# Kernel optimization log

Hardware: AMD Instinct MI355X
Metric: run time of the kernel (lower is better)

Reference implementation:

```python
import jax, jax.numpy as jnp
import numpy as np

T, E = 16384, 1024   # frames, feature dim (WavLM-Large)
M, K = 8, 512        # number of kmeans models, clusters per model


def setup_inputs() -> dict:
    key = jax.random.key(0)
    k1, k2, k3 = jax.random.split(key, 3)
    emb = jax.random.normal(k1, (1, T, E), dtype=jnp.float32)
    centroids = jax.random.normal(k2, (M, K, E), dtype=jnp.float32)
    # per-frame random kmeans model choice (stride=1): replaces random.randint in the loop
    model_idx = jax.random.randint(k3, (T,), 0, M, dtype=jnp.int32)
    return {"emb": emb, "centroids": centroids, "model_idx": model_idx}


def reference(emb, centroids, model_idx):
    # emb: [1,T,E], centroids: [M,K,E], model_idx: [T] in [0,M)
    x = emb[0]  # [T,E]
    # squared euclidean distance from every frame to every centroid of every model
    # (argmin over squared dist == argmin over cdist)
    x_sq = jnp.sum(x * x, axis=-1)                      # [T]
    c_sq = jnp.sum(centroids * centroids, axis=-1)      # [M,K]
    dots = jnp.einsum('te,mke->tmk', x, centroids)      # [T,M,K]
    d_all = x_sq[:, None, None] - 2.0 * dots + c_sq[None, :, :]  # [T,M,K]
    # select the randomly chosen model's distances per frame
    d = jnp.take_along_axis(d_all, model_idx[:, None, None].astype(jnp.int32), axis=1)[:, 0, :]  # [T,K]
    codes = jnp.argmin(d, axis=-1)                      # [T]
    # embedding lookup: the quantizer's emb maps cluster id -> centroid vector
    out = centroids[model_idx, codes]                   # [T,E]
    return out[None]  # [1,T,E]
```

## Files before the change

kernel.cpp:

```cpp
#include <hip/hip_runtime.h>


#define T_FRAMES 16384
#define E_DIM    1024
#define M_MODELS 8
#define K_CLUST  512

#define FPB 32
#define NCH 8

typedef __bf16 bf16x8 __attribute__((ext_vector_type(8)));
typedef float  floatx16 __attribute__((ext_vector_type(16)));

__device__ __forceinline__ bf16x8 cvt8(const float4 a, const float4 b) {
  bf16x8 h;
  h[0] = (__bf16)a.x; h[1] = (__bf16)a.y; h[2] = (__bf16)a.z; h[3] = (__bf16)a.w;
  h[4] = (__bf16)b.x; h[5] = (__bf16)b.y; h[6] = (__bf16)b.z; h[7] = (__bf16)b.w;
  return h;
}

__global__ __launch_bounds__(256) void k_csq(const float* __restrict__ cent,
                                             double* __restrict__ csq64) {
  const int row = blockIdx.x * 4 + (threadIdx.x >> 6);
  const int lane = threadIdx.x & 63;
  const float* p = cent + (size_t)row * E_DIM;
  double s = 0.0;
#pragma unroll
  for (int i = 0; i < 16; ++i) {
    const float v = p[lane + i * 64];
    s += (double)v * (double)v;
  }
#pragma unroll
  for (int m = 32; m >= 1; m >>= 1) s += __shfl_xor(s, m, 64);
  if (lane == 0) csq64[row] = s;
}

__global__ __launch_bounds__(256) void k_cvt(const float* __restrict__ cent,
                                             float* __restrict__ out) {
  const int b = blockIdx.x;
  const int m = b >> 6;
  const int cg = (b >> 2) & 15;
  const int q = b & 3;
  const int tid = threadIdx.x;
  const int ci = tid & 31;
  const int gk0 = q * 32 + (tid >> 5) * 4;
  const int B32 = (m * 16 + cg) * 32;
  const float* src = cent + ((size_t)(m * K_CLUST + cg * 32 + ci)) * E_DIM;
#pragma unroll
  for (int j = 0; j < 4; ++j) {
    const int gk = gk0 + j;
    const float4 a = *(const float4*)(src + gk * 8);
    const float4 bb = *(const float4*)(src + gk * 8 + 4);
    const size_t foff = (size_t)(B32 + (gk >> 2)) * 1024 + 512 +
                        ((gk & 3) * 32 + ci) * 4;
    *(bf16x8*)(out + foff) = cvt8(a, bb);
  }
}

__global__ __launch_bounds__(256) void k_hist(const int* __restrict__ midx,
                                              int* __restrict__ hist) {
  __shared__ int h[M_MODELS * 33];
  const int tid = threadIdx.x;
  for (int i = tid; i < M_MODELS * 33; i += 256) h[i] = 0;
  __syncthreads();
  const int m = midx[blockIdx.x * 256 + tid];
  atomicAdd(&h[m * 33 + (tid & 31)], 1);
  __syncthreads();
  if (tid < M_MODELS) {
    int s = 0;
    for (int j = 0; j < 32; ++j) s += h[tid * 33 + j];
    hist[blockIdx.x * M_MODELS + tid] = s;
  }
}

__global__ __launch_bounds__(256) void k_scatter(const int* __restrict__ midx,
                                                 const int* __restrict__ hist,
                                                 int* __restrict__ order,
                                                 int* __restrict__ offs) {
  __shared__ int h2[64 * M_MODELS];
  __shared__ int cur[M_MODELS];
  const int tid = threadIdx.x;
  h2[tid] = hist[tid];
  h2[tid + 256] = hist[tid + 256];
  __syncthreads();
  if (tid < M_MODELS) {
    int tot_before = 0;
    for (int mp = 0; mp < tid; ++mp)
      for (int b = 0; b < 64; ++b) tot_before += h2[b * M_MODELS + mp];
    int prior = 0;
    for (int b = 0; b < (int)blockIdx.x; ++b) prior += h2[b * M_MODELS + tid];
    cur[tid] = tot_before + prior;
  }
  if (blockIdx.x == 0 && tid <= M_MODELS) {
    int o = 0;
    for (int mp = 0; mp < tid; ++mp)
      for (int b = 0; b < 64; ++b) o += h2[b * M_MODELS + mp];
    offs[tid] = o;
  }
  __syncthreads();
  const int f = blockIdx.x * 256 + tid;
  const int pos = atomicAdd(&cur[midx[f]], 1);
  order[pos] = f;
}

__global__ __launch_bounds__(256, 2) void k_dist(const float* __restrict__ emb,
                                                 const float* __restrict__ cent,
                                                 const double* __restrict__ csq64,
                                                 const int* __restrict__ order,
                                                 const int* __restrict__ offs,
                                                 float* __restrict__ out) {
  const int m = blockIdx.x;
  const int o0 = offs[m];
  const int cnt = offs[m + 1] - o0;
  const int start = blockIdx.y * FPB;
  if (start >= cnt) return;
  const int nvalid = min(FPB, cnt - start);

  __shared__ __align__(16) __bf16 A_l[2 * 16 * FPB * 8];
  __shared__ int rows_l[FPB];
  __shared__ float wmin_s[4][FPB];
  __shared__ int wcol_s[4][FPB];
  __shared__ float gmin_s[FPB];
  __shared__ int cnt_s[FPB];
  __shared__ int cand_s[FPB][32];

  const int tid = threadIdx.x;
  const int l = tid & 63;
  const int w = tid >> 6;
  const int ln = l & 31;
  const int lh = l >> 5;

  if (tid < FPB) rows_l[tid] = order[o0 + start + min(tid, nvalid - 1)];
  __syncthreads();

  const int s_row = tid & 31;
  const int s_gp = tid >> 5;
  const float4* emb4 = (const float4*)emb;
  const size_t arow4 = (size_t)rows_l[s_row] * (E_DIM / 4);

  float4 pa[4];
#pragma unroll
  for (int j = 0; j < 4; ++j) pa[j] = emb4[arow4 + s_gp * 4 + j];
  *(bf16x8*)(A_l + ((s_gp * 2 + 0) * FPB + s_row) * 8) = cvt8(pa[0], pa[1]);
  *(bf16x8*)(A_l + ((s_gp * 2 + 1) * FPB + s_row) * 8) = cvt8(pa[2], pa[3]);

  const char* bbase[4];
#pragma unroll
  for (int ct = 0; ct < 4; ++ct) {
    const int cg = w * 4 + ct;
    bbase[ct] = (const char*)out + (size_t)(m * 16 + cg) * 131072 + 2048 + l * 16;
  }
#define LOADB(ct, kb) (*(const bf16x8*)(bbase[ct] + (((kb) >> 1) << 12) + (((kb) & 1) << 10)))

  bf16x8 bR[4][4];
#pragma unroll
  for (int d = 0; d < 4; ++d)
#pragma unroll
    for (int ct = 0; ct < 4; ++ct) bR[d][ct] = LOADB(ct, d);

  floatx16 acc[4] = {};

  for (int c = 0; c < NCH; ++c) {
    __syncthreads();
    const int buf = (c & 1) * 16;
    if (c + 1 < NCH) {
#pragma unroll
      for (int j = 0; j < 4; ++j) pa[j] = emb4[arow4 + (c + 1) * 32 + s_gp * 4 + j];
    }
#pragma unroll
    for (int jj = 0; jj < 8; ++jj) {
      const int kb = c * 8 + jj;
      const int p = kb & 3;
      const bf16x8 a0 = *(const bf16x8*)(A_l + ((buf + jj * 2 + lh) * FPB + ln) * 8);
#pragma unroll
      for (int ct = 0; ct < 4; ++ct)
        acc[ct] = __builtin_amdgcn_mfma_f32_32x32x16_bf16(a0, bR[p][ct], acc[ct], 0, 0, 0);
      if (kb + 4 < 64) {
#pragma unroll
        for (int ct = 0; ct < 4; ++ct) bR[p][ct] = LOADB(ct, kb + 4);
      }
    }
    if (c + 1 < NCH) {
      const int nbuf = ((c + 1) & 1) * 16;
      *(bf16x8*)(A_l + ((nbuf + s_gp * 2 + 0) * FPB + s_row) * 8) = cvt8(pa[0], pa[1]);
      *(bf16x8*)(A_l + ((nbuf + s_gp * 2 + 1) * FPB + s_row) * 8) = cvt8(pa[2], pa[3]);
    }
  }
#undef LOADB

  float cs[4];
#pragma unroll
  for (int ct = 0; ct < 4; ++ct)
    cs[ct] = (float)csq64[m * K_CLUST + w * 128 + ct * 32 + ln];

#pragma unroll
  for (int r = 0; r < 16; ++r) {
    const int fr = (r & 3) + 8 * (r >> 2) + 4 * lh;
    float bm = cs[0] - 2.0f * acc[0][r];
    int bc = w * 128 + ln;
#pragma unroll
    for (int ct = 1; ct < 4; ++ct) {
      const float s = cs[ct] - 2.0f * acc[ct][r];
      if (s < bm) { bm = s; bc = w * 128 + ct * 32 + ln; }
    }
#pragma unroll
    for (int sh = 1; sh <= 16; sh <<= 1) {
      const float om = __shfl_xor(bm, sh, 64);
      const int oc = __shfl_xor(bc, sh, 64);
      if (om < bm || (om == bm && oc < bc)) { bm = om; bc = oc; }
    }
    if (ln == 0) { wmin_s[w][fr] = bm; wcol_s[w][fr] = bc; }
  }
  __syncthreads();

  if (tid < FPB) {
    float g = wmin_s[0][tid];
    int gc = wcol_s[0][tid];
#pragma unroll
    for (int w2 = 1; w2 < 4; ++w2) {
      const float v = wmin_s[w2][tid];
      const int vc = wcol_s[w2][tid];
      if (v < g || (v == g && vc < gc)) { g = v; gc = vc; }
    }
    gmin_s[tid] = g;
    cnt_s[tid] = 0;
  }
  __syncthreads();

#pragma unroll
  for (int r = 0; r < 16; ++r) {
    const int fr = (r & 3) + 8 * (r >> 2) + 4 * lh;
    const float thr = gmin_s[fr] + 3.0f;
#pragma unroll
    for (int ct = 0; ct < 4; ++ct) {
      const float s = cs[ct] - 2.0f * acc[ct][r];
      if (s < thr) {
        const int ix = atomicAdd(&cnt_s[fr], 1);
        if (ix < 32) cand_s[fr][ix] = w * 128 + ct * 32 + ln;
      }
    }
  }
  __syncthreads();

  for (int i = 0; i < 8; ++i) {
    const int f = w * 8 + i;
    const int t = rows_l[f];
    const int n = min(cnt_s[f], 32);
    int code;
    if (n == 1) {
      code = cand_s[f][0];
    } else {
      float4 xv[4];
#pragma unroll
      for (int q = 0; q < 4; ++q) xv[q] = emb4[(size_t)t * (E_DIM / 4) + q * 64 + l];
      double bd = 1e300;
      int bi = 1 << 30;
      for (int j = 0; j < n; ++j) {
        const int cc = cand_s[f][j];
        const float4* crow4 = (const float4*)(cent + ((size_t)(m * K_CLUST + cc)) * E_DIM);
        double s = 0.0;
#pragma unroll
        for (int q = 0; q < 4; ++q) {
          const float4 cv = crow4[q * 64 + l];
          s += (double)xv[q].x * cv.x + (double)xv[q].y * cv.y +
               (double)xv[q].z * cv.z + (double)xv[q].w * cv.w;
        }
#pragma unroll
        for (int sh = 32; sh >= 1; sh >>= 1) s += __shfl_xor(s, sh, 64);
        const double d = csq64[m * K_CLUST + cc] - 2.0 * s;
        if (d < bd || (d == bd && cc < bi)) { bd = d; bi = cc; }
      }
      code = bi;
    }
    if (l == 0) *(int*)(out + (size_t)t * E_DIM) = code;
  }
}

__global__ __launch_bounds__(256) void k_gather(const float* __restrict__ cent,
                                                const int* __restrict__ midx,
                                                float* __restrict__ out) {
  const int t = blockIdx.x * 4 + (threadIdx.x >> 6);
  const int l = threadIdx.x & 63;
  float* drow = out + (size_t)t * E_DIM;
  const int code = *(const int*)drow;
  const int m = midx[t];
  const float4* src = (const float4*)(cent + ((size_t)(m * K_CLUST + code)) * E_DIM);
  float4* dst = (float4*)drow;
#pragma unroll
  for (int q = 0; q < 4; ++q) dst[q * 64 + l] = src[q * 64 + l];
}

extern "C" void kernel_launch(void* const* d_in, const int* in_sizes, int n_in,
                              void* d_out, int out_size, void* d_ws, size_t ws_size,
                              hipStream_t stream) {
  const float* emb = (const float*)d_in[0];
  const float* cent = (const float*)d_in[1];
  const int* midx = (const int*)d_in[2];
  float* out = (float*)d_out;

  char* ws = (char*)d_ws;
  double* csq64 = (double*)(ws + 0);
  int* hist = (int*)(ws + 32768);
  int* offs = (int*)(ws + 34816);
  int* order = (int*)(ws + 34880);

  hipLaunchKernelGGL(k_cvt, dim3(512), dim3(256), 0, stream, cent, out);
  hipLaunchKernelGGL(k_csq, dim3(1024), dim3(256), 0, stream, cent, csq64);
  hipLaunchKernelGGL(k_hist, dim3(64), dim3(256), 0, stream, midx, hist);
  hipLaunchKernelGGL(k_scatter, dim3(64), dim3(256), 0, stream, midx, hist, order, offs);
  hipLaunchKernelGGL(k_dist, dim3(M_MODELS, 80), dim3(256), 0, stream,
                     emb, cent, csq64, order, offs, out);
  hipLaunchKernelGGL(k_gather, dim3(T_FRAMES / 4), dim3(256), 0, stream,
                     cent, midx, out);
}
```

Before: 206.2 us.

## Split distance kernel work across 8 waves with 64 clusters each

```diff
diff --git a/kernel.cpp b/kernel.cpp
--- a/kernel.cpp
+++ b/kernel.cpp
@@ -103,7 +103,7 @@
   order[pos] = f;
 }
 
-__global__ __launch_bounds__(256, 2) void k_dist(const float* __restrict__ emb,
+__global__ __launch_bounds__(512, 4) void k_dist(const float* __restrict__ emb,
                                                  const float* __restrict__ cent,
                                                  const double* __restrict__ csq64,
                                                  const int* __restrict__ order,
@@ -118,8 +118,8 @@
 
   __shared__ __align__(16) __bf16 A_l[2 * 16 * FPB * 8];
   __shared__ int rows_l[FPB];
-  __shared__ float wmin_s[4][FPB];
-  __shared__ int wcol_s[4][FPB];
+  __shared__ float wmin_s[8][FPB];
+  __shared__ int wcol_s[8][FPB];
   __shared__ float gmin_s[FPB];
   __shared__ int cnt_s[FPB];
   __shared__ int cand_s[FPB][32];
@@ -134,74 +134,70 @@
   __syncthreads();
 
   const int s_row = tid & 31;
-  const int s_gp = tid >> 5;
+  const int s_g = tid >> 5;
   const float4* emb4 = (const float4*)emb;
   const size_t arow4 = (size_t)rows_l[s_row] * (E_DIM / 4);
 
-  float4 pa[4];
-#pragma unroll
-  for (int j = 0; j < 4; ++j) pa[j] = emb4[arow4 + s_gp * 4 + j];
-  *(bf16x8*)(A_l + ((s_gp * 2 + 0) * FPB + s_row) * 8) = cvt8(pa[0], pa[1]);
-  *(bf16x8*)(A_l + ((s_gp * 2 + 1) * FPB + s_row) * 8) = cvt8(pa[2], pa[3]);
-
-  const char* bbase[4];
-#pragma unroll
-  for (int ct = 0; ct < 4; ++ct) {
-    const int cg = w * 4 + ct;
+  float4 pa[2];
+  pa[0] = emb4[arow4 + s_g * 2 + 0];
+  pa[1] = emb4[arow4 + s_g * 2 + 1];
+  *(bf16x8*)(A_l + ((s_g)*FPB + s_row) * 8) = cvt8(pa[0], pa[1]);
+
+  const char* bbase[2];
+#pragma unroll
+  for (int ct = 0; ct < 2; ++ct) {
+    const int cg = w * 2 + ct;
     bbase[ct] = (const char*)out + (size_t)(m * 16 + cg) * 131072 + 2048 + l * 16;
   }
 #define LOADB(ct, kb) (*(const bf16x8*)(bbase[ct] + (((kb) >> 1) << 12) + (((kb) & 1) << 10)))
 
-  bf16x8 bR[4][4];
+  bf16x8 bR[4][2];
 #pragma unroll
   for (int d = 0; d < 4; ++d)
 #pragma unroll
-    for (int ct = 0; ct < 4; ++ct) bR[d][ct] = LOADB(ct, d);
-
-  floatx16 acc[4] = {};
+    for (int ct = 0; ct < 2; ++ct) bR[d][ct] = LOADB(ct, d);
+
+  floatx16 acc[2] = {};
 
   for (int c = 0; c < NCH; ++c) {
     __syncthreads();
     const int buf = (c & 1) * 16;
     if (c + 1 < NCH) {
-#pragma unroll
-      for (int j = 0; j < 4; ++j) pa[j] = emb4[arow4 + (c + 1) * 32 + s_gp * 4 + j];
+      pa[0] = emb4[arow4 + (c + 1) * 32 + s_g * 2 + 0];
+      pa[1] = emb4[arow4 + (c + 1) * 32 + s_g * 2 + 1];
     }
 #pragma unroll
     for (int jj = 0; jj < 8; ++jj) {
       const int kb = c * 8 + jj;
       const int p = kb & 3;
       const bf16x8 a0 = *(const bf16x8*)(A_l + ((buf + jj * 2 + lh) * FPB + ln) * 8);
-#pragma unroll
-      for (int ct = 0; ct < 4; ++ct)
-        acc[ct] = __builtin_amdgcn_mfma_f32_32x32x16_bf16(a0, bR[p][ct], acc[ct], 0, 0, 0);
+      acc[0] = __builtin_amdgcn_mfma_f32_32x32x16_bf16(a0, bR[p][0], acc[0], 0, 0, 0);
+      acc[1] = __builtin_amdgcn_mfma_f32_32x32x16_bf16(a0, bR[p][1], acc[1], 0, 0, 0);
       if (kb + 4 < 64) {
-#pragma unroll
-        for (int ct = 0; ct < 4; ++ct) bR[p][ct] = LOADB(ct, kb + 4);
+        bR[p][0] = LOADB(0, kb + 4);
+        bR[p][1] = LOADB(1, kb + 4);
       }
     }
     if (c + 1 < NCH) {
       const int nbuf = ((c + 1) & 1) * 16;
-      *(bf16x8*)(A_l + ((nbuf + s_gp * 2 + 0) * FPB + s_row) * 8) = cvt8(pa[0], pa[1]);
-      *(bf16x8*)(A_l + ((nbuf + s_gp * 2 + 1) * FPB + s_row) * 8) = cvt8(pa[2], pa[3]);
+      *(bf16x8*)(A_l + ((nbuf + s_g) * FPB + s_row) * 8) = cvt8(pa[0], pa[1]);
     }
   }
 #undef LOADB
 
-  float cs[4];
-#pragma unroll
-  for (int ct = 0; ct < 4; ++ct)
-    cs[ct] = (float)csq64[m * K_CLUST + w * 128 + ct * 32 + ln];
+  float cs[2];
+#pragma unroll
+  for (int ct = 0; ct < 2; ++ct)
+    cs[ct] = (float)csq64[m * K_CLUST + w * 64 + ct * 32 + ln];
 
 #pragma unroll
   for (int r = 0; r < 16; ++r) {
     const int fr = (r & 3) + 8 * (r >> 2) + 4 * lh;
     float bm = cs[0] - 2.0f * acc[0][r];
-    int bc = w * 128 + ln;
-#pragma unroll
-    for (int ct = 1; ct < 4; ++ct) {
-      const float s = cs[ct] - 2.0f * acc[ct][r];
-      if (s < bm) { bm = s; bc = w * 128 + ct * 32 + ln; }
+    int bc = w * 64 + ln;
+    {
+      const float s = cs[1] - 2.0f * acc[1][r];
+      if (s < bm) { bm = s; bc = w * 64 + 32 + ln; }
     }
 #pragma unroll
     for (int sh = 1; sh <= 16; sh <<= 1) {
@@ -217,7 +213,7 @@
     float g = wmin_s[0][tid];
     int gc = wcol_s[0][tid];
 #pragma unroll
-    for (int w2 = 1; w2 < 4; ++w2) {
+    for (int w2 = 1; w2 < 8; ++w2) {
       const float v = wmin_s[w2][tid];
       const int vc = wcol_s[w2][tid];
       if (v < g || (v == g && vc < gc)) { g = v; gc = vc; }
@@ -232,18 +228,18 @@
     const int fr = (r & 3) + 8 * (r >> 2) + 4 * lh;
     const float thr = gmin_s[fr] + 3.0f;
 #pragma unroll
-    for (int ct = 0; ct < 4; ++ct) {
+    for (int ct = 0; ct < 2; ++ct) {
       const float s = cs[ct] - 2.0f * acc[ct][r];
       if (s < thr) {
         const int ix = atomicAdd(&cnt_s[fr], 1);
-        if (ix < 32) cand_s[fr][ix] = w * 128 + ct * 32 + ln;
+        if (ix < 32) cand_s[fr][ix] = w * 64 + ct * 32 + ln;
       }
     }
   }
   __syncthreads();
 
-  for (int i = 0; i < 8; ++i) {
-    const int f = w * 8 + i;
+  for (int i = 0; i < 4; ++i) {
+    const int f = w * 4 + i;
     const int t = rows_l[f];
     const int n = min(cnt_s[f], 32);
     int code;
@@ -308,7 +304,7 @@
   hipLaunchKernelGGL(k_csq, dim3(1024), dim3(256), 0, stream, cent, csq64);
   hipLaunchKernelGGL(k_hist, dim3(64), dim3(256), 0, stream, midx, hist);
   hipLaunchKernelGGL(k_scatter, dim3(64), dim3(256), 0, stream, midx, hist, order, offs);
-  hipLaunchKernelGGL(k_dist, dim3(M_MODELS, 80), dim3(256), 0, stream,
+  hipLaunchKernelGGL(k_dist, dim3(M_MODELS, 80), dim3(512), 0, stream,
                      emb, cent, csq64, order, offs, out);
   hipLaunchKernelGGL(k_gather, dim3(T_FRAMES / 4), dim3(256), 0, stream,
                      cent, midx, out);
```

After: 205.6 us. Within noise of the previous version (-0.3%).
